# Optimization experiments

Hardware: AMD Instinct MI355X
Metric: run time of the kernel (lower is better)

## Reference

```python
import jax, jax.numpy as jnp
import numpy as np

T, B, F = 256, 128, 1024


def setup_inputs() -> dict:
    key = jax.random.key(0)
    ks = jax.random.split(key, 6)
    x = jax.random.normal(ks[0], (T, B, F), dtype=jnp.float32)
    terminations = jax.random.randint(ks[1], (T, B), 0, 2).astype(jnp.int32)
    c0 = jax.random.normal(ks[2], (B, F), dtype=jnp.float32)
    h0 = jax.random.normal(ks[3], (B, F), dtype=jnp.float32)
    # OptimizedLSTMCell fused kernels: input->4F (no bias), hidden->4F (bias)
    Wi = jax.random.normal(ks[4], (F, 4 * F), dtype=jnp.float32) / np.sqrt(F).astype(np.float32)
    Wh = jax.random.normal(ks[5], (F, 4 * F), dtype=jnp.float32) / np.sqrt(F).astype(np.float32)
    b = jnp.zeros((4 * F,), dtype=jnp.float32)
    return {"x": x, "terminations": terminations, "c0": c0, "h0": h0,
            "Wi": Wi, "Wh": Wh, "b": b}


def reference(x, terminations, c0, h0, Wi, Wh, b):
    Bz, Fz = c0.shape
    xs = x.reshape(-1, Bz, Fz)              # (T, B, F)
    terms = terminations.reshape(-1, Bz)    # (T, B)
    # Precompute input projection for all timesteps (big batched GEMM)
    xW = jnp.einsum('tbf,fg->tbg', xs, Wi)  # (T, B, 4F)

    def step(carry, inp):
        c, h = carry
        xw, t = inp
        # termination-based state reset (terminate != 0 -> zero carry)
        mask = (t != 0)[:, None]
        c = jnp.where(mask, jnp.zeros_like(c), c)
        h = jnp.where(mask, jnp.zeros_like(h), h)
        gates = xw + h @ Wh + b               # (B, 4F)
        i, f, g, o = jnp.split(gates, 4, axis=-1)  # flax gate order i,f,g,o
        new_c = jax.nn.sigmoid(f) * c + jax.nn.sigmoid(i) * jnp.tanh(g)
        new_h = jax.nn.sigmoid(o) * jnp.tanh(new_c)
        return (new_c, new_h), new_h

    (fc, fh), y = jax.lax.scan(step, (c0, h0), (xW, terms))
    if xs.shape[0] == 1:
        y = jnp.squeeze(y, axis=0)
    return (y, fc, fh)
```

## Files before the change

### kernel.cpp

```cpp
#include <hip/hip_runtime.h>

#define T_DIM 256
#define B_DIM 128
#define F_DIM 1024
#define G_DIM 4096
#define LA    8
#define XWR   16

typedef short bf8   __attribute__((ext_vector_type(8)));
typedef float f32x4 __attribute__((ext_vector_type(4)));
typedef unsigned int u32x4 __attribute__((ext_vector_type(4)));
typedef unsigned long long u64;

#define OFF_CTRL 0ull
#define SZ_CTRL  131072ull
#define OFF_WIP  (SZ_CTRL)
#define SZ_WP    (8ull<<20)
#define OFF_WHP  (OFF_WIP+SZ_WP)
#define OFF_HR   (OFF_WHP+SZ_WP)
#define SZ_HR    (2ull*262144ull)
#define OFF_XW   (OFF_HR+SZ_HR)
#define SZ_XW    ((unsigned long long)XWR*1048576ull)
#define OFF_XPK  (OFF_XW+SZ_XW)
#define WS_MIN   OFF_XPK
#define WS_BIG   (OFF_XPK + 64ull*1048576ull)
#define CO_ARR   2048
#define CO_LTAG  4096
#define CO_BTAG  40960

__device__ __forceinline__ unsigned short f2bf(float v) {
  union { float f; unsigned u; } c; c.f = v;
  return (unsigned short)((c.u + 0x7fffu + ((c.u >> 16) & 1u)) >> 16);
}
__device__ __forceinline__ float bf2f(unsigned short u) {
  union { unsigned i; float f; } c; c.i = ((unsigned)u) << 16; return c.f;
}
__device__ __forceinline__ float sigm(float x)  { return 1.f / (1.f + __expf(-x)); }
__device__ __forceinline__ float tanh_(float x) { return 1.f - 2.f / (1.f + __expf(2.f * x)); }
__device__ __forceinline__ bf8 as_bf8(u32x4 v) { union { u32x4 a; bf8 b; } u; u.a = v; return u.b; }
__device__ __forceinline__ bf8 cvt_bf8(float4 a, float4 b) {
  union { unsigned short s[8]; bf8 v; } u;
  u.s[0]=f2bf(a.x); u.s[1]=f2bf(a.y); u.s[2]=f2bf(a.z); u.s[3]=f2bf(a.w);
  u.s[4]=f2bf(b.x); u.s[5]=f2bf(b.y); u.s[6]=f2bf(b.z); u.s[7]=f2bf(b.w);
  return u.v;
}
__device__ __forceinline__ unsigned ldflag(const void* p, bool loc) {
  unsigned v;
  if (loc) asm volatile("global_load_dword %0, %1, off sc0\n\ts_waitcnt vmcnt(0)" : "=v"(v) : "v"(p));
  else     asm volatile("global_load_dword %0, %1, off sc0 sc1\n\ts_waitcnt vmcnt(0)" : "=v"(v) : "v"(p));
  return v;
}
__device__ __forceinline__ void stflag(void* p, unsigned v, bool loc) {
  if (loc) *(volatile unsigned*)p = v;
  else __hip_atomic_store((unsigned*)p, v, __ATOMIC_RELAXED, __HIP_MEMORY_SCOPE_AGENT);
}
__device__ __forceinline__ void ld4(u32x4& a, u32x4& b, u32x4& c, u32x4& d,
                                    const void* p0, const void* p1, const void* p2, const void* p3, bool loc) {
  if (loc)
    asm volatile("global_load_dwordx4 %0, %4, off sc0\n\t"
                 "global_load_dwordx4 %1, %5, off sc0\n\t"
                 "global_load_dwordx4 %2, %6, off sc0\n\t"
                 "global_load_dwordx4 %3, %7, off sc0\n\t"
                 "s_waitcnt vmcnt(0)"
                 : "=&v"(a), "=&v"(b), "=&v"(c), "=&v"(d)
                 : "v"(p0), "v"(p1), "v"(p2), "v"(p3));
  else
    asm volatile("global_load_dwordx4 %0, %4, off sc0 sc1\n\t"
                 "global_load_dwordx4 %1, %5, off sc0 sc1\n\t"
                 "global_load_dwordx4 %2, %6, off sc0 sc1\n\t"
                 "global_load_dwordx4 %3, %7, off sc0 sc1\n\t"
                 "s_waitcnt vmcnt(0)"
                 : "=&v"(a), "=&v"(b), "=&v"(c), "=&v"(d)
                 : "v"(p0), "v"(p1), "v"(p2), "v"(p3));
}
__device__ __forceinline__ void st_short_sc1(void* p, unsigned v) {
  asm volatile("global_store_short %0, %1, off sc1" :: "v"(p), "v"(v) : "memory");
}

__global__ __launch_bounds__(256) void pack_w(const float* __restrict__ Wi, const float* __restrict__ Wh,
                                              unsigned short* __restrict__ wip, unsigned short* __restrict__ whp) {
  int gid = blockIdx.x * 256 + threadIdx.x;
  const float* src = (gid >= 524288) ? Wh : Wi;
  unsigned short* dst = (gid >= 524288) ? whp : wip;
  int r = gid & 524287, nt = r >> 11, kt = (r >> 6) & 31, l = r & 63;
  int col = nt * 16 + (l & 15), k0 = kt * 32 + ((l >> 4) << 3);
  bf8 v8;
#pragma unroll
  for (int j = 0; j < 8; ++j) v8[j] = (short)f2bf(src[(size_t)(k0 + j) * G_DIM + col]);
  *reinterpret_cast<bf8*>(dst + (size_t)r * 8) = v8;
}

__global__ __launch_bounds__(256) void pack_h(const float* __restrict__ h0, unsigned short* __restrict__ hr) {
  int i = blockIdx.x * 256 + threadIdx.x;
  hr[i] = f2bf(h0[i]);
}

__global__ __launch_bounds__(256) void pack_x(const float* __restrict__ x, unsigned short* __restrict__ xpk) {
  int gid = blockIdx.x * 256 + threadIdx.x;
  const float4* s = reinterpret_cast<const float4*>(x + (size_t)gid * 8);
  *reinterpret_cast<bf8*>(xpk + (size_t)gid * 8) = cvt_bf8(s[0], s[1]);
}

struct SmT {
  u32x4 wi[32][64];
  u32x4 hst[32][64];
  float gates[4][16][33];
  int   info[8];
  char  pad[20480];
};

__global__ __launch_bounds__(512, 2) void lstm_scan(
    const float* __restrict__ x, const unsigned short* __restrict__ xpk, int useXpk,
    const unsigned short* __restrict__ wip, const unsigned short* __restrict__ whp,
    unsigned short* __restrict__ hring, unsigned short* __restrict__ xwring,
    const float* __restrict__ bias, const int* __restrict__ term,
    const float* __restrict__ c0, float* __restrict__ out, char* __restrict__ ctrl) {
  __shared__ SmT sm;

  const int wg = blockIdx.x, tid = threadIdx.x;
  const int wv = tid >> 6, lane = tid & 63, oct = lane >> 4;

  if (tid == 0) {
    unsigned xcc = __builtin_amdgcn_s_getreg(63508) & 7u;
    unsigned slot = __hip_atomic_fetch_add((unsigned*)(ctrl + (size_t)xcc * 128), 1u,
                                           __ATOMIC_RELAXED, __HIP_MEMORY_SCOPE_AGENT);
    sm.info[0] = (int)xcc; sm.info[1] = (int)slot;
    __hip_atomic_fetch_add((unsigned*)(ctrl + CO_ARR), 1u, __ATOMIC_RELEASE, __HIP_MEMORY_SCOPE_AGENT);
  }
  __syncthreads();
  if (tid == 0) {
    while (__hip_atomic_load((unsigned*)(ctrl + CO_ARR), __ATOMIC_ACQUIRE, __HIP_MEMORY_SCOPE_AGENT) < 256u)
      __builtin_amdgcn_s_sleep(8);
    int ok = 1;
    for (int g = 0; g < 8; ++g)
      ok &= (__hip_atomic_load((unsigned*)(ctrl + (size_t)g * 128), __ATOMIC_RELAXED, __HIP_MEMORY_SCOPE_AGENT) == 32u);
    sm.info[2] = ok;
  }
  __syncthreads();
  const bool loc = (sm.info[2] != 0);
  const int G = loc ? sm.info[0] : (wg >> 5);
  const int R = loc ? sm.info[1] : (wg & 31);
  char* ltag = ctrl + CO_LTAG;
  char* btag = ctrl + CO_BTAG;

  const int nt_bg = G * 32 + R;
  {
    int jb = tid >> 6, l6 = tid & 63;
#pragma unroll
    for (int k = 0; k < 4; ++k) {
      int j = jb + 8 * k;
      sm.wi[j][l6] = *reinterpret_cast<const u32x4*>(wip + ((size_t)(nt_bg * 32 + j) * 64 + l6) * 8);
    }
  }
  const int gt = wv >> 1, hf = wv & 1;
  const int ntS = gt * 64 + R * 2 + hf;
  bf8 wh[32];
#pragma unroll
  for (int k = 0; k < 32; ++k)
    wh[k] = *reinterpret_cast<const bf8*>(whp + ((size_t)(ntS * 32 + k) * 64 + lane) * 8);
#pragma unroll
  for (int k = 0; k < 32; ++k) asm volatile("" : "+v"(wh[k]));
  __syncthreads();

  const int erow = tid >> 5, ecol = tid & 31;
  const int grow = G * 16 + erow, fcol = R * 32 + ecol;
  float b4[4];
#pragma unroll
  for (int g = 0; g < 4; ++g) b4[g] = bias[g * F_DIM + fcol];
  float c_reg = c0[(size_t)grow * F_DIM + fcol];

  const int g_bg = nt_bg >> 6, cb_bg = (nt_bg & 63) * 16;
  float* fc = out + (size_t)T_DIM * B_DIM * F_DIM;
  float* fh = fc + (size_t)B_DIM * F_DIM;

  auto bg_pass = [&](int s) {
    f32x4 acc = {0, 0, 0, 0};
    if (useXpk) {
      const unsigned short* xb = xpk + (size_t)s * 131072 + (size_t)(wv * 16 + (lane & 15)) * 1024 + oct * 8;
#pragma unroll
      for (int j = 0; j < 32; ++j) {
        bf8 A = *reinterpret_cast<const bf8*>(xb + j * 32);
        acc = __builtin_amdgcn_mfma_f32_16x16x32_bf16(A, as_bf8(sm.wi[j][lane]), acc, 0, 0, 0);
      }
    } else {
      const float* xb = x + (size_t)s * 131072 + (size_t)(wv * 16 + (lane & 15)) * 1024 + oct * 8;
#pragma unroll
      for (int j = 0; j < 32; ++j) {
        float4 a = *reinterpret_cast<const float4*>(xb + j * 32);
        float4 b = *reinterpret_cast<const float4*>(xb + j * 32 + 4);
        acc = __builtin_amdgcn_mfma_f32_16x16x32_bf16(cvt_bf8(a, b), as_bf8(sm.wi[j][lane]), acc, 0, 0, 0);
      }
    }
    unsigned short* slot = xwring + (size_t)(s % XWR) * 524288;
#pragma unroll
    for (int r = 0; r < 4; ++r) {
      int row = wv * 16 + oct * 4 + r, col = cb_bg + (lane & 15);
      st_short_sc1(slot + ((size_t)(row * 1024 + col) * 4 + g_bg), (unsigned)f2bf(acc[r]));
    }
  };

  for (int s = 0; s < LA; ++s) bg_pass(s);
  __syncthreads();
  if (tid == 0) stflag(btag + (size_t)(G * 32 + R) * 128, 1u, false);

#pragma unroll 1
  for (int t = 0; t < T_DIM; ++t) {
    if (wv == 0) {
      unsigned tg = (t >= LA - 1) ? (unsigned)(t - LA + 2) : 1u;
      for (;;) {
        unsigned f0 = ldflag(btag + (size_t)lane * 128, false);
        unsigned f1 = ldflag(btag + (size_t)(lane + 64) * 128, false);
        unsigned f2 = ldflag(btag + (size_t)(lane + 128) * 128, false);
        unsigned f3 = ldflag(btag + (size_t)(lane + 192) * 128, false);
        if (__all((f0 >= tg) & (f1 >= tg) & (f2 >= tg) & (f3 >= tg))) break;
        __builtin_amdgcn_s_sleep(2);
      }
      if (t > 0) {
        const void* lp = ltag + (size_t)(G * 32 + (lane & 31)) * 128;
        for (;;) {
          unsigned f = ldflag(lp, loc);
          if (__all((lane >= 32) | (f >= (unsigned)(t + 1)))) break;
          __builtin_amdgcn_s_sleep(1);
        }
      }
    }
    __syncthreads();

    u64 xwv = __hip_atomic_load(
        reinterpret_cast<const u64*>(xwring + (size_t)(t % XWR) * 524288) + ((size_t)grow * 1024 + fcol),
        __ATOMIC_RELAXED, __HIP_MEMORY_SCOPE_AGENT);

    {
      int row = tid & 15, o2 = (tid >> 4) & 3, l6 = tid & 63, jb = tid >> 6;
      const unsigned short* hs = hring + (size_t)(t & 1) * 131072 + (size_t)(G * 16 + row) * 1024 + o2 * 8;
      int trm = term[t * B_DIM + G * 16 + row];
      u32x4 v0, v1, v2, v3;
      ld4(v0, v1, v2, v3, hs + (jb) * 32, hs + (jb + 8) * 32, hs + (jb + 16) * 32, hs + (jb + 24) * 32, loc);
      u32x4 zz = {0, 0, 0, 0};
      if (trm) { v0 = zz; v1 = zz; v2 = zz; v3 = zz; }
      sm.hst[jb][l6] = v0; sm.hst[jb + 8][l6] = v1; sm.hst[jb + 16][l6] = v2; sm.hst[jb + 24][l6] = v3;
    }
    __syncthreads();

    f32x4 acc = {0, 0, 0, 0};
#pragma unroll
    for (int j = 0; j < 32; ++j)
      acc = __builtin_amdgcn_mfma_f32_16x16x32_bf16(as_bf8(sm.hst[j][lane]), wh[j], acc, 0, 0, 0);
#pragma unroll
    for (int r = 0; r < 4; ++r) sm.gates[gt][oct * 4 + r][hf * 16 + (lane & 15)] = acc[r];
    __syncthreads();

    int trmE = term[t * B_DIM + grow];
    float hx[4];
#pragma unroll
    for (int g = 0; g < 4; ++g)
      hx[g] = bf2f((unsigned short)(xwv >> (16 * g))) + b4[g] + sm.gates[g][erow][ecol];
    float cp = trmE ? 0.f : c_reg;
    float cn = sigm(hx[1]) * cp + sigm(hx[0]) * tanh_(hx[2]);
    float hn = sigm(hx[3]) * tanh_(cn);
    c_reg = cn;
    {
      unsigned my = f2bf(hn);
      unsigned nb = (unsigned)__shfl_xor((int)my, 1, 64);
      if (!(ecol & 1)) {
        unsigned pk = my | (nb << 16);
        void* dst = hring + (size_t)((t + 1) & 1) * 131072 + (size_t)grow * 1024 + (fcol & ~1);
        if (loc) *(volatile unsigned*)dst = pk;
        else __hip_atomic_store((unsigned*)dst, pk, __ATOMIC_RELAXED, __HIP_MEMORY_SCOPE_AGENT);
      }
    }
    __syncthreads();
    if (tid == 0) stflag(ltag + (size_t)(G * 32 + R) * 128, (unsigned)(t + 2), loc);

    out[((size_t)t * B_DIM + grow) * F_DIM + fcol] = hn;
    if (t == T_DIM - 1) {
      fc[(size_t)grow * F_DIM + fcol] = cn;
      fh[(size_t)grow * F_DIM + fcol] = hn;
    }

    if (t + LA < T_DIM) bg_pass(t + LA);
    __syncthreads();
    if (tid == 0) stflag(btag + (size_t)(G * 32 + R) * 128, (unsigned)(t + 2), false);
  }
}

extern "C" void kernel_launch(void* const* d_in, const int* in_sizes, int n_in,
                              void* d_out, int out_size, void* d_ws, size_t ws_size,
                              hipStream_t stream) {
  const float* x    = (const float*)d_in[0];
  const int*   term = (const int*)d_in[1];
  const float* c0   = (const float*)d_in[2];
  const float* h0   = (const float*)d_in[3];
  const float* Wi   = (const float*)d_in[4];
  const float* Wh   = (const float*)d_in[5];
  const float* bias = (const float*)d_in[6];
  float* out = (float*)d_out;
  char*  ws  = (char*)d_ws;

  if (ws_size < WS_MIN) return;
  int useXpk = (ws_size >= WS_BIG) ? 1 : 0;

  char*           ctrl = ws + OFF_CTRL;
  unsigned short* wip  = (unsigned short*)(ws + OFF_WIP);
  unsigned short* whp  = (unsigned short*)(ws + OFF_WHP);
  unsigned short* hr   = (unsigned short*)(ws + OFF_HR);
  unsigned short* xw   = (unsigned short*)(ws + OFF_XW);
  unsigned short* xpk  = (unsigned short*)(ws + OFF_XPK);

  hipMemsetAsync(ctrl, 0, SZ_CTRL, stream);
  pack_w<<<dim3(4096), dim3(256), 0, stream>>>(Wi, Wh, wip, whp);
  pack_h<<<dim3(512),  dim3(256), 0, stream>>>(h0, hr);
  if (useXpk) pack_x<<<dim3(16384), dim3(256), 0, stream>>>(x, xpk);
  lstm_scan<<<dim3(256), dim3(512), 0, stream>>>(x, xpk, useXpk, wip, whp, hr, xw,
                                                 bias, term, c0, out, ctrl);
}
```

Measured before the change: 3.199 ms.

## Store xW ring gate-planar with packed dword stores and defer background-ready flag

Changes the precomputed input-projection ring from gate-interleaved layout to four gate-major planes. Adjacent lanes pair their bf16 results through a shuffle, so the background GEMM writes dwords instead of scattered shorts. The recurrent step now reads four dwords instead of one 64-bit word. The background-pass completion flag moves to the start of the next step, after the barrier, which removes one __syncthreads per timestep. It also indexes the flag by nt_bg instead of G*32+R, which relies on nt_bg being defined consistently in the unseen code.

```diff
diff --git a/kernel.cpp b/kernel.cpp
--- a/kernel.cpp
+++ b/kernel.cpp
@@ -20,7 +20,7 @@
 #define OFF_HR   (OFF_WHP+SZ_WP)
 #define SZ_HR    (2ull*262144ull)
 #define OFF_XW   (OFF_HR+SZ_HR)
-#define SZ_XW    ((unsigned long long)XWR*1048576ull)
+#define SZ_XW    ((u64)XWR*1048576ull)
 #define OFF_XPK  (OFF_XW+SZ_XW)
 #define WS_MIN   OFF_XPK
 #define WS_BIG   (OFF_XPK + 64ull*1048576ull)
@@ -73,8 +73,8 @@
                  : "=&v"(a), "=&v"(b), "=&v"(c), "=&v"(d)
                  : "v"(p0), "v"(p1), "v"(p2), "v"(p3));
 }
-__device__ __forceinline__ void st_short_sc1(void* p, unsigned v) {
-  asm volatile("global_store_short %0, %1, off sc1" :: "v"(p), "v"(v) : "memory");
+__device__ __forceinline__ void st_dword_sc1(void* p, unsigned v) {
+  asm volatile("global_store_dword %0, %1, off sc1" :: "v"(p), "v"(v) : "memory");
 }
 
 __global__ __launch_bounds__(256) void pack_w(const float* __restrict__ Wi, const float* __restrict__ Wh,
@@ -191,17 +191,22 @@
         acc = __builtin_amdgcn_mfma_f32_16x16x32_bf16(cvt_bf8(a, b), as_bf8(sm.wi[j][lane]), acc, 0, 0, 0);
       }
     }
-    unsigned short* slot = xwring + (size_t)(s % XWR) * 524288;
+    unsigned short* slotp = xwring + (size_t)(s % XWR) * 524288 + (size_t)g_bg * 131072;
 #pragma unroll
     for (int r = 0; r < 4; ++r) {
-      int row = wv * 16 + oct * 4 + r, col = cb_bg + (lane & 15);
-      st_short_sc1(slot + ((size_t)(row * 1024 + col) * 4 + g_bg), (unsigned)f2bf(acc[r]));
+      int row = wv * 16 + oct * 4 + r;
+      unsigned my = f2bf(acc[r]);
+      unsigned nb = (unsigned)__shfl_xor((int)my, 1, 64);
+      if (!(lane & 1)) {
+        unsigned pk = my | (nb << 16);
+        st_dword_sc1(slotp + (size_t)row * 1024 + cb_bg + ((lane & 15) & ~1), pk);
+      }
     }
   };
 
   for (int s = 0; s < LA; ++s) bg_pass(s);
   __syncthreads();
-  if (tid == 0) stflag(btag + (size_t)(G * 32 + R) * 128, 1u, false);
+  if (tid == 0) stflag(btag + (size_t)nt_bg * 128, 1u, false);
 
 #pragma unroll 1
   for (int t = 0; t < T_DIM; ++t) {
@@ -226,9 +231,17 @@
     }
     __syncthreads();
 
-    u64 xwv = __hip_atomic_load(
-        reinterpret_cast<const u64*>(xwring + (size_t)(t % XWR) * 524288) + ((size_t)grow * 1024 + fcol),
-        __ATOMIC_RELAXED, __HIP_MEMORY_SCOPE_AGENT);
+    if (tid == 0 && t >= 1 && (t - 1 + LA) < T_DIM)
+      stflag(btag + (size_t)nt_bg * 128, (unsigned)(t + 1), false);
+
+    unsigned xg[4];
+    {
+      const unsigned short* xwb = xwring + (size_t)(t % XWR) * 524288 + (size_t)grow * 1024 + (fcol & ~1);
+#pragma unroll
+      for (int g = 0; g < 4; ++g)
+        xg[g] = __hip_atomic_load(reinterpret_cast<const unsigned*>(xwb + (size_t)g * 131072),
+                                  __ATOMIC_RELAXED, __HIP_MEMORY_SCOPE_AGENT);
+    }
 
     {
       int row = tid & 15, o2 = (tid >> 4) & 3, l6 = tid & 63, jb = tid >> 6;
@@ -254,7 +267,7 @@
     float hx[4];
 #pragma unroll
     for (int g = 0; g < 4; ++g)
-      hx[g] = bf2f((unsigned short)(xwv >> (16 * g))) + b4[g] + sm.gates[g][erow][ecol];
+      hx[g] = bf2f((unsigned short)(xg[g] >> ((fcol & 1) * 16))) + b4[g] + sm.gates[g][erow][ecol];
     float cp = trmE ? 0.f : c_reg;
     float cn = sigm(hx[1]) * cp + sigm(hx[0]) * tanh_(hx[2]);
     float hn = sigm(hx[3]) * tanh_(cn);
@@ -279,8 +292,6 @@
     }
 
     if (t + LA < T_DIM) bg_pass(t + LA);
-    __syncthreads();
-    if (tid == 0) stflag(btag + (size_t)(G * 32 + R) * 128, (unsigned)(t + 2), false);
   }
 }
 
```

New measurement: 3.100 ms. -3.1%, faster.
